# Optimization experiments

Measured on AMD Instinct MI355X. Metric: run time of the kernel, lower is better.

## Reference

```python
import jax, jax.numpy as jnp
import numpy as np

NUM_HEADS = 8
SIZE_Q = 512
SIZE_K = 512
SIZE_V = 512
B, S = 2, 2048


def setup_inputs() -> dict:
    key = jax.random.key(0)
    ks = jax.random.split(key, 16)
    Hk = SIZE_K  # num_heads * head_size_k
    Hv = SIZE_V  # num_heads * head_size_v
    inp = {
        "k": jax.random.normal(ks[0], (B, S, SIZE_K), jnp.float32),
        "v": jax.random.normal(ks[1], (B, S, SIZE_V), jnp.float32),
        "q": jax.random.normal(ks[2], (B, S, SIZE_Q), jnp.float32),
        "mask": jax.random.randint(ks[3], (S, S), 0, 2).astype(jnp.bool_),
        "spatial_bias": jax.random.normal(ks[4], (1, NUM_HEADS, S, S), jnp.float32),
        # Linear params stored as [in, out]; y = x @ W + b
        "Wq": jax.random.normal(ks[5], (SIZE_Q, Hk), jnp.float32) / np.sqrt(SIZE_Q),
        "bq": jnp.zeros((Hk,), jnp.float32),
        "Wk": jax.random.normal(ks[6], (SIZE_K, Hk), jnp.float32) / np.sqrt(SIZE_K),
        "bk": jnp.zeros((Hk,), jnp.float32),
        "Wv": jax.random.normal(ks[7], (SIZE_V, Hv), jnp.float32) / np.sqrt(SIZE_V),
        "bv": jnp.zeros((Hv,), jnp.float32),
        "Wo": jax.random.normal(ks[8], (Hv, SIZE_V), jnp.float32) / np.sqrt(Hv),
        "bo": jnp.zeros((SIZE_V,), jnp.float32),
    }
    return inp


def reference(k, v, q, mask, spatial_bias, Wq, bq, Wk, bk, Wv, bv, Wo, bo):
    batch, sk = k.shape[0], k.shape[1]
    sq = q.shape[1]
    hdk = Wk.shape[1] // NUM_HEADS
    hdv = Wv.shape[1] // NUM_HEADS
    # QKV projections -> [B, H, S, hd]
    kp = (k @ Wk + bk).reshape(batch, sk, NUM_HEADS, hdk).transpose(0, 2, 1, 3)
    vp = (v @ Wv + bv).reshape(batch, sk, NUM_HEADS, hdv).transpose(0, 2, 1, 3)
    qp = (q @ Wq + bq).reshape(batch, sq, NUM_HEADS, hdk).transpose(0, 2, 1, 3)
    qp = qp / jnp.sqrt(jnp.asarray(hdk, qp.dtype))
    # Scores with additive spatial bias and boolean mask (2D mask -> [1,1,S,S])
    scores = jnp.einsum("bhqd,bhkd->bhqk", qp, kp) + spatial_bias
    scores = jnp.where(mask[None, None, :, :], scores, -jnp.inf)
    attn = jax.nn.softmax(scores, axis=-1)  # dropout=0 (eval)
    ctx = jnp.einsum("bhqk,bhkd->bhqd", attn, vp)
    ctx = ctx.transpose(0, 2, 1, 3).reshape(batch, sq, NUM_HEADS * hdv)
    return ctx @ Wo + bo
```

## Files before the change

kernel.cpp:

```cpp
#include <hip/hip_runtime.h>
#include <hip/hip_bf16.h>

#define S_LEN 2048
#define NH 8
#define HD 64
#define CH 512
#define NEG_BIG (-3.0e38f)

typedef __bf16 bf16;
typedef bf16 bf16x8 __attribute__((ext_vector_type(8)));
typedef bf16 bf16x4 __attribute__((ext_vector_type(4)));
typedef float floatx4 __attribute__((ext_vector_type(4)));

__global__ void detect_mask_kernel(const unsigned char* __restrict__ mb,
                                   int* __restrict__ flag_out) {
    __shared__ int s1, s3;
    if (threadIdx.x == 0) { s1 = 0; s3 = 0; }
    __syncthreads();
    int any1 = 0, any3 = 0;
    int base = threadIdx.x * 16;
    for (int i = base; i < base + 16; ++i) {
        unsigned char bch = mb[i];
        int m = i & 3;
        if (bch != 0) {
            if (m == 1) any1 = 1;
            if (m == 2 || m == 3) any3 = 1;
        }
    }
    if (any1) atomicOr(&s1, 1);
    if (any3) atomicOr(&s3, 1);
    __syncthreads();
    if (threadIdx.x == 0) {
        int f = 0;
        if (s1) f = 1;
        else if (s3) f = 2;
        *flag_out = f;
    }
}

__global__ __launch_bounds__(256) void prep_weights_kernel(
    const float* __restrict__ Wq, const float* __restrict__ Wk,
    const float* __restrict__ Wv, const float* __restrict__ Wo,
    bf16* __restrict__ WThi, bf16* __restrict__ WTlo)
{
    __shared__ float tile[64][65];
    const int t = threadIdx.x;
    const int n0 = blockIdx.x * 64;
    const int k0 = blockIdx.y * 64;
    const int mat = blockIdx.z;
    const float* W = (mat == 0) ? Wq : (mat == 1) ? Wk : (mat == 2) ? Wv : Wo;
    bf16* hi = WThi + (size_t)mat * (CH * CH);
    bf16* lo = WTlo + (size_t)mat * (CH * CH);
#pragma unroll
    for (int i = 0; i < 4; ++i) {
        int row = (t >> 4) + 16 * i;
        int c4 = (t & 15) << 2;
        float4 f = *(const float4*)(W + (size_t)(k0 + row) * CH + n0 + c4);
        tile[row][c4 + 0] = f.x; tile[row][c4 + 1] = f.y;
        tile[row][c4 + 2] = f.z; tile[row][c4 + 3] = f.w;
    }
    __syncthreads();
#pragma unroll
    for (int i = 0; i < 4; ++i) {
        int nr = (t >> 4) + 16 * i;
        int k4 = (t & 15) << 2;
        bf16x4 h, l;
#pragma unroll
        for (int j = 0; j < 4; ++j) {
            float x = tile[k4 + j][nr];
            bf16 hv = (bf16)x;
            h[j] = hv;
            l[j] = (bf16)(x - (float)hv);
        }
        *(bf16x4*)(hi + (size_t)(n0 + nr) * CH + k0 + k4) = h;
        *(bf16x4*)(lo + (size_t)(n0 + nr) * CH + k0 + k4) = l;
    }
}

__device__ __forceinline__ void gemm_bf16_tile(
    bf16* __restrict__ As_hi, bf16* __restrict__ As_lo,
    bf16* __restrict__ Bs_hi, bf16* __restrict__ Bs_lo,
    const float* __restrict__ IN, const bf16* __restrict__ WThi,
    const bf16* __restrict__ WTlo, const float* __restrict__ BI,
    float* __restrict__ OUT, float scale, int mode)
{
    const int t = threadIdx.x;
    const int w = t >> 6;
    const int lane = t & 63;
    const int m16 = lane & 15;
    const int quad = lane >> 4;
    const int m0 = blockIdx.y * 128;
    const int n0 = blockIdx.x * 128;

    const int arow = t >> 1;
    const int akc  = (t & 1) << 4;

    floatx4 acc[2][8];
#pragma unroll
    for (int mi = 0; mi < 2; ++mi)
#pragma unroll
        for (int ni = 0; ni < 8; ++ni) {
            acc[mi][ni][0] = 0.f; acc[mi][ni][1] = 0.f;
            acc[mi][ni][2] = 0.f; acc[mi][ni][3] = 0.f;
        }

    float4 af[4];
    bf16x8 pbh[2], pbl[2];

    auto loadA = [&](int k0) {
        const float* p = IN + (size_t)(m0 + arow) * CH + k0 + akc;
        af[0] = ((const float4*)p)[0];
        af[1] = ((const float4*)p)[1];
        af[2] = ((const float4*)p)[2];
        af[3] = ((const float4*)p)[3];
    };
    auto loadB = [&](int k0) {
        const bf16* ph = WThi + (size_t)(n0 + arow) * CH + k0 + akc;
        const bf16* pl = WTlo + (size_t)(n0 + arow) * CH + k0 + akc;
        pbh[0] = ((const bf16x8*)ph)[0]; pbh[1] = ((const bf16x8*)ph)[1];
        pbl[0] = ((const bf16x8*)pl)[0]; pbl[1] = ((const bf16x8*)pl)[1];
    };
    auto stage = [&]() {
#pragma unroll
        for (int hh = 0; hh < 2; ++hh) {
            bf16x8 h, l;
#pragma unroll
            for (int j = 0; j < 8; ++j) {
                float x = ((const float*)&af[2 * hh])[j];
                bf16 hv = (bf16)x;
                h[j] = hv;
                l[j] = (bf16)(x - (float)hv);
            }
            *(bf16x8*)&As_hi[arow * 40 + akc + 8 * hh] = h;
            *(bf16x8*)&As_lo[arow * 40 + akc + 8 * hh] = l;
        }
        *(bf16x8*)&Bs_hi[arow * 40 + akc + 0] = pbh[0];
        *(bf16x8*)&Bs_hi[arow * 40 + akc + 8] = pbh[1];
        *(bf16x8*)&Bs_lo[arow * 40 + akc + 0] = pbl[0];
        *(bf16x8*)&Bs_lo[arow * 40 + akc + 8] = pbl[1];
    };

    loadA(0); loadB(0);
    for (int ks = 0; ks < CH / 32; ++ks) {
        __syncthreads();
        stage();
        __syncthreads();
        if (ks + 1 < CH / 32) { loadA(32 * (ks + 1)); loadB(32 * (ks + 1)); }

        bf16x8 bh[8], bl[8];
#pragma unroll
        for (int ni = 0; ni < 8; ++ni) {
            bh[ni] = *(const bf16x8*)&Bs_hi[(16 * ni + m16) * 40 + 8 * quad];
            bl[ni] = *(const bf16x8*)&Bs_lo[(16 * ni + m16) * 40 + 8 * quad];
        }
#pragma unroll
        for (int mi = 0; mi < 2; ++mi) {
            bf16x8 ah = *(const bf16x8*)&As_hi[(32 * w + 16 * mi + m16) * 40 + 8 * quad];
            bf16x8 al = *(const bf16x8*)&As_lo[(32 * w + 16 * mi + m16) * 40 + 8 * quad];
#pragma unroll
            for (int ni = 0; ni < 8; ++ni) {
                acc[mi][ni] = __builtin_amdgcn_mfma_f32_16x16x32_bf16(ah, bh[ni], acc[mi][ni], 0, 0, 0);
                acc[mi][ni] = __builtin_amdgcn_mfma_f32_16x16x32_bf16(ah, bl[ni], acc[mi][ni], 0, 0, 0);
                acc[mi][ni] = __builtin_amdgcn_mfma_f32_16x16x32_bf16(al, bh[ni], acc[mi][ni], 0, 0, 0);
            }
        }
    }

#pragma unroll
    for (int mi = 0; mi < 2; ++mi) {
#pragma unroll
        for (int r = 0; r < 4; ++r) {
            int row = m0 + 32 * w + 16 * mi + 4 * quad + r;
            int bb = row >> 11;
            int ss = row & (S_LEN - 1);
#pragma unroll
            for (int ni = 0; ni < 8; ++ni) {
                int col = n0 + 16 * ni + m16;
                float v = (acc[mi][ni][r] + BI[col]) * scale;
                if (mode == 0) {
                    int hh = col >> 6, dd = col & 63;
                    OUT[(((size_t)bb * NH + hh) * S_LEN + ss) * HD + dd] = v;
                } else if (mode == 1) {
                    int hh = col >> 6, dd = col & 63;
                    OUT[(((size_t)bb * NH + hh) * HD + dd) * S_LEN + ss] = v;
                } else {
                    OUT[(size_t)row * CH + col] = v;
                }
            }
        }
    }
}

__global__ __launch_bounds__(256, 2) void qkv_gemm_kernel(
    const float* __restrict__ q_in, const float* __restrict__ k_in,
    const float* __restrict__ v_in,
    const bf16* __restrict__ WThi, const bf16* __restrict__ WTlo,
    const float* __restrict__ bq, const float* __restrict__ bk,
    const float* __restrict__ bv,
    float* __restrict__ qp, float* __restrict__ kp, float* __restrict__ vpT)
{
    __shared__ __attribute__((aligned(16))) bf16 As_hi[128 * 40];
    __shared__ __attribute__((aligned(16))) bf16 As_lo[128 * 40];
    __shared__ __attribute__((aligned(16))) bf16 Bs_hi[128 * 40];
    __shared__ __attribute__((aligned(16))) bf16 Bs_lo[128 * 40];
    int z = blockIdx.z;
    if (z == 0)
        gemm_bf16_tile(As_hi, As_lo, Bs_hi, Bs_lo, q_in,
                       WThi, WTlo, bq, qp, 0.125f, 0);
    else if (z == 1)
        gemm_bf16_tile(As_hi, As_lo, Bs_hi, Bs_lo, k_in,
                       WThi + (size_t)CH * CH, WTlo + (size_t)CH * CH, bk, kp, 1.0f, 0);
    else
        gemm_bf16_tile(As_hi, As_lo, Bs_hi, Bs_lo, v_in,
                       WThi + (size_t)2 * CH * CH, WTlo + (size_t)2 * CH * CH, bv, vpT, 1.0f, 1);
}

__global__ __launch_bounds__(256, 2) void out_gemm_kernel(
    const float* __restrict__ ctx,
    const bf16* __restrict__ WThi, const bf16* __restrict__ WTlo,
    const float* __restrict__ bo, float* __restrict__ out)
{
    __shared__ __attribute__((aligned(16))) bf16 As_hi[128 * 40];
    __shared__ __attribute__((aligned(16))) bf16 As_lo[128 * 40];
    __shared__ __attribute__((aligned(16))) bf16 Bs_hi[128 * 40];
    __shared__ __attribute__((aligned(16))) bf16 Bs_lo[128 * 40];
    gemm_bf16_tile(As_hi, As_lo, Bs_hi, Bs_lo, ctx,
                   WThi + (size_t)3 * CH * CH, WTlo + (size_t)3 * CH * CH, bo, out, 1.0f, 2);
}

__global__ __launch_bounds__(256, 2) void attn_kernel(
    const float* __restrict__ qp, const float* __restrict__ kp,
    const float* __restrict__ vpT, const float* __restrict__ bias,
    const void* __restrict__ mask, const int* __restrict__ flagp,
    float* __restrict__ ctxb)
{
    __shared__ __attribute__((aligned(16))) bf16 Kbf[64 * 72];
    __shared__ __attribute__((aligned(16))) bf16 VsT[64 * 72];
    __shared__ __attribute__((aligned(16))) bf16 Pbf[64 * 72];
    __shared__ __attribute__((aligned(16))) float sbias[64 * 68];

    const int t    = threadIdx.x;
    const int w    = t >> 6;
    const int lane = t & 63;
    const int m    = lane & 15;
    const int quad = lane >> 4;
    const int q0   = blockIdx.x * 64;
    const int h    = blockIdx.y;
    const int b    = blockIdx.z;
    const int bh   = b * NH + h;
    const int flag = *flagp;

    bf16x8 qf[2];
    {
        const float* qrow =
            qp + ((size_t)bh * S_LEN + q0 + 16 * w + m) * HD + 8 * quad;
#pragma unroll
        for (int c = 0; c < 2; ++c) {
            float4 f0 = *(const float4*)(qrow + 32 * c);
            float4 f1 = *(const float4*)(qrow + 32 * c + 4);
            bf16x8 v;
            v[0] = (bf16)f0.x; v[1] = (bf16)f0.y; v[2] = (bf16)f0.z; v[3] = (bf16)f0.w;
            v[4] = (bf16)f1.x; v[5] = (bf16)f1.y; v[6] = (bf16)f1.z; v[7] = (bf16)f1.w;
            qf[c] = v;
        }
    }

    floatx4 ctx[4];
    float mrow[4], lrow[4];
#pragma unroll
    for (int tt = 0; tt < 4; ++tt) { ctx[tt][0]=0.f; ctx[tt][1]=0.f; ctx[tt][2]=0.f; ctx[tt][3]=0.f; }
#pragma unroll
    for (int r = 0; r < 4; ++r) { mrow[r] = NEG_BIG; lrow[r] = 0.f; }

    float4 kreg[4], vreg[4], breg[4];
    uint4  mreg[4];

    auto prefetch = [&](int k0) {
#pragma unroll
        for (int i = 0; i < 4; ++i) {
            int fl  = t + 256 * i;
            int row = fl >> 4;
            int c4  = (fl & 15) << 2;
            kreg[i] = *(const float4*)(kp  + ((size_t)bh * S_LEN + k0 + row) * HD + c4);
            vreg[i] = *(const float4*)(vpT + ((size_t)bh * HD + row) * S_LEN + k0 + c4);
            int grow = q0 + row;
            breg[i] = *(const float4*)(bias + ((size_t)h * S_LEN + grow) * S_LEN + k0 + c4);
            size_t mi0 = (size_t)grow * S_LEN + k0 + c4;
            if (flag == 1)
                mreg[i].x = *(const unsigned int*)((const unsigned char*)mask + mi0);
            else
                mreg[i] = *(const uint4*)((const unsigned int*)mask + mi0);
        }
    };
    auto stage = [&]() {
#pragma unroll
        for (int i = 0; i < 4; ++i) {
            int fl  = t + 256 * i;
            int row = fl >> 4;
            int c4  = (fl & 15) << 2;
            float4 kf = kreg[i], vf = vreg[i], bf = breg[i];
            bf16x4 kv, vv;
            kv[0] = (bf16)kf.x; kv[1] = (bf16)kf.y; kv[2] = (bf16)kf.z; kv[3] = (bf16)kf.w;
            vv[0] = (bf16)vf.x; vv[1] = (bf16)vf.y; vv[2] = (bf16)vf.z; vv[3] = (bf16)vf.w;
            *(bf16x4*)&Kbf[row * 72 + c4] = kv;
            *(bf16x4*)&VsT[row * 72 + c4] = vv;
            unsigned mj0, mj1, mj2, mj3;
            if (flag == 1) {
                unsigned mx = mreg[i].x;
                mj0 = mx & 255u; mj1 = (mx >> 8) & 255u;
                mj2 = (mx >> 16) & 255u; mj3 = mx >> 24;
            } else {
                mj0 = mreg[i].x; mj1 = mreg[i].y; mj2 = mreg[i].z; mj3 = mreg[i].w;
            }
            float4 sb;
            sb.x = mj0 ? bf.x : NEG_BIG;
            sb.y = mj1 ? bf.y : NEG_BIG;
            sb.z = mj2 ? bf.z : NEG_BIG;
            sb.w = mj3 ? bf.w : NEG_BIG;
            *(float4*)&sbias[row * 68 + c4] = sb;
        }
    };

    prefetch(0);
    for (int k0 = 0; k0 < S_LEN; k0 += 64) {
        __syncthreads();
        stage();
        __syncthreads();
        if (k0 + 64 < S_LEN) prefetch(k0 + 64);

        floatx4 sc[4];
#pragma unroll
        for (int tt = 0; tt < 4; ++tt) { sc[tt][0]=0.f; sc[tt][1]=0.f; sc[tt][2]=0.f; sc[tt][3]=0.f; }
#pragma unroll
        for (int st = 0; st < 2; ++st)
#pragma unroll
            for (int tt = 0; tt < 4; ++tt) {
                bf16x8 kf = *(const bf16x8*)&Kbf[(16 * tt + m) * 72 + 8 * quad + 32 * st];
                sc[tt] = __builtin_amdgcn_mfma_f32_16x16x32_bf16(qf[st], kf, sc[tt], 0, 0, 0);
            }

        float alpha[4];
#pragma unroll
        for (int r = 0; r < 4; ++r) {
            int lrowq = 16 * w + 4 * quad + r;
            float s[4];
#pragma unroll
            for (int tt = 0; tt < 4; ++tt)
                s[tt] = sc[tt][r] + sbias[lrowq * 68 + 16 * tt + m];
            float mx = fmaxf(fmaxf(s[0], s[1]), fmaxf(s[2], s[3]));
            mx = fmaxf(mx, __shfl_xor(mx, 1));
            mx = fmaxf(mx, __shfl_xor(mx, 2));
            mx = fmaxf(mx, __shfl_xor(mx, 4));
            mx = fmaxf(mx, __shfl_xor(mx, 8));
            float mnew = fmaxf(mrow[r], mx);
            float al = __expf(mrow[r] - mnew);
            float ls = 0.f;
#pragma unroll
            for (int tt = 0; tt < 4; ++tt) {
                float p = (s[tt] <= -1e37f) ? 0.f : __expf(s[tt] - mnew);
                ls += p;
                Pbf[lrowq * 72 + 16 * tt + m] = (bf16)p;
            }
            ls += __shfl_xor(ls, 1);
            ls += __shfl_xor(ls, 2);
            ls += __shfl_xor(ls, 4);
            ls += __shfl_xor(ls, 8);
            lrow[r] = lrow[r] * al + ls;
            mrow[r] = mnew;
            alpha[r] = al;
        }
#pragma unroll
        for (int tt = 0; tt < 4; ++tt)
#pragma unroll
            for (int r = 0; r < 4; ++r) ctx[tt][r] *= alpha[r];

#pragma unroll
        for (int st = 0; st < 2; ++st) {
            bf16x8 pf = *(const bf16x8*)&Pbf[(16 * w + m) * 72 + 8 * quad + 32 * st];
#pragma unroll
            for (int tt = 0; tt < 4; ++tt) {
                bf16x8 vf = *(const bf16x8*)&VsT[(16 * tt + m) * 72 + 8 * quad + 32 * st];
                ctx[tt] = __builtin_amdgcn_mfma_f32_16x16x32_bf16(pf, vf, ctx[tt], 0, 0, 0);
            }
        }
    }

#pragma unroll
    for (int r = 0; r < 4; ++r) {
        float inv = lrow[r] > 0.f ? 1.f / lrow[r] : 0.f;
        int grow = q0 + 16 * w + 4 * quad + r;
#pragma unroll
        for (int tt = 0; tt < 4; ++tt) {
            ctxb[((size_t)b * S_LEN + grow) * CH + h * HD + 16 * tt + m] =
                ctx[tt][r] * inv;
        }
    }
}

extern "C" void kernel_launch(void* const* d_in, const int* in_sizes, int n_in,
                              void* d_out, int out_size, void* d_ws, size_t ws_size,
                              hipStream_t stream) {
    const float* k_in = (const float*)d_in[0];
    const float* v_in = (const float*)d_in[1];
    const float* q_in = (const float*)d_in[2];
    const void*  mask = d_in[3];
    const float* bias = (const float*)d_in[4];
    const float* Wq = (const float*)d_in[5];
    const float* bq = (const float*)d_in[6];
    const float* Wk = (const float*)d_in[7];
    const float* bk = (const float*)d_in[8];
    const float* Wv = (const float*)d_in[9];
    const float* bv = (const float*)d_in[10];
    const float* Wo = (const float*)d_in[11];
    const float* bo = (const float*)d_in[12];
    float* out = (float*)d_out;

    float* wsf = (float*)d_ws;
    float* qp  = wsf;
    float* kp  = wsf + 2097152;
    float* vpT = wsf + 4194304;
    float* ctx = wsf + 6291456;
    bf16* WThi = (bf16*)(wsf + 8388608);
    bf16* WTlo = WThi + (size_t)4 * CH * CH;
    int*  flag = (int*)(WTlo + (size_t)4 * CH * CH);

    detect_mask_kernel<<<1, 256, 0, stream>>>((const unsigned char*)mask, flag);
    prep_weights_kernel<<<dim3(8, 8, 4), 256, 0, stream>>>(
        Wq, Wk, Wv, Wo, WThi, WTlo);
    qkv_gemm_kernel<<<dim3(4, 32, 3), 256, 0, stream>>>(
        q_in, k_in, v_in, WThi, WTlo, bq, bk, bv, qp, kp, vpT);
    attn_kernel<<<dim3(32, 8, 2), 256, 0, stream>>>(
        qp, kp, vpT, bias, mask, flag, ctx);
    out_gemm_kernel<<<dim3(4, 32, 1), 256, 0, stream>>>(
        ctx, WThi, WTlo, bo, out);
}
```

Before: 385.7 us.

## Store projections in bf16, premask bias to fp16, split ctx in attention

QKV projections now write bf16 outputs, with the V transpose staged through LDS for coalesced stores. A new prep kernel folds the boolean mask into the spatial bias and stores it as fp16 with a finite sentinel. The attention kernel loads compact bf16/f16 tiles, runs at higher occupancy, and emits the hi/lo bf16 split of ctx consumed directly by the output GEMM. This cuts fp32 traffic and in-loop conversion work, at the cost of an extra full pass over the bias tensor and reduced bias precision.

```diff
diff --git a/kernel.cpp b/kernel.cpp
--- a/kernel.cpp
+++ b/kernel.cpp
@@ -5,11 +5,15 @@
 #define NH 8
 #define HD 64
 #define CH 512
-#define NEG_BIG (-3.0e38f)
+#define NEG_INIT (-1.0e30f)
+#define MASK_SENT (-30000.0f)
 
 typedef __bf16 bf16;
 typedef bf16 bf16x8 __attribute__((ext_vector_type(8)));
 typedef bf16 bf16x4 __attribute__((ext_vector_type(4)));
+typedef _Float16 f16;
+typedef f16 f16x4 __attribute__((ext_vector_type(4)));
+typedef f16 f16x8 __attribute__((ext_vector_type(8)));
 typedef float floatx4 __attribute__((ext_vector_type(4)));
 
 __global__ void detect_mask_kernel(const unsigned char* __restrict__ mb,
@@ -77,18 +81,53 @@
     }
 }
 
-__device__ __forceinline__ void gemm_bf16_tile(
-    bf16* __restrict__ As_hi, bf16* __restrict__ As_lo,
-    bf16* __restrict__ Bs_hi, bf16* __restrict__ Bs_lo,
-    const float* __restrict__ IN, const bf16* __restrict__ WThi,
-    const bf16* __restrict__ WTlo, const float* __restrict__ BI,
-    float* __restrict__ OUT, float scale, int mode)
-{
+__global__ __launch_bounds__(256) void prep_sbias_kernel(
+    const float* __restrict__ bias, const void* __restrict__ mask,
+    const int* __restrict__ flagp, f16* __restrict__ sbias)
+{
+    int idx = blockIdx.x * 256 + threadIdx.x;
+    int i4 = idx << 2;
+    int q = i4 >> 11;
+    int k = i4 & (S_LEN - 1);
+    int flag = *flagp;
+    unsigned mj[4];
+    if (flag == 1) {
+        unsigned mx = *(const unsigned*)((const unsigned char*)mask + (size_t)q * S_LEN + k);
+        mj[0] = mx & 255u; mj[1] = (mx >> 8) & 255u;
+        mj[2] = (mx >> 16) & 255u; mj[3] = mx >> 24;
+    } else {
+        uint4 mx = *(const uint4*)((const unsigned*)mask + (size_t)q * S_LEN + k);
+        mj[0] = mx.x; mj[1] = mx.y; mj[2] = mx.z; mj[3] = mx.w;
+    }
+#pragma unroll
+    for (int h = 0; h < NH; ++h) {
+        float4 bv = *(const float4*)(bias + ((size_t)h * S_LEN + q) * S_LEN + k);
+        f16x4 sb;
+        sb[0] = (f16)(mj[0] ? bv.x : MASK_SENT);
+        sb[1] = (f16)(mj[1] ? bv.y : MASK_SENT);
+        sb[2] = (f16)(mj[2] ? bv.z : MASK_SENT);
+        sb[3] = (f16)(mj[3] ? bv.w : MASK_SENT);
+        *(f16x4*)(sbias + ((size_t)h * S_LEN + q) * S_LEN + k) = sb;
+    }
+}
+
+template <int MODE, bool ASPLIT>
+__device__ __forceinline__ void gemm_core(
+    bf16* __restrict__ SMEM,
+    const float* __restrict__ INF,
+    const bf16* __restrict__ INH, const bf16* __restrict__ INL,
+    const bf16* __restrict__ WThi, const bf16* __restrict__ WTlo,
+    const float* __restrict__ BI, void* __restrict__ OUT, float scale)
+{
+    bf16* As_hi = SMEM;
+    bf16* As_lo = SMEM + 128 * 40;
+    bf16* Bs_hi = SMEM + 2 * 128 * 40;
+    bf16* Bs_lo = SMEM + 3 * 128 * 40;
+
     const int t = threadIdx.x;
     const int w = t >> 6;
-    const int lane = t & 63;
-    const int m16 = lane & 15;
-    const int quad = lane >> 4;
+    const int m16 = (t & 63) & 15;
+    const int quad = (t & 63) >> 4;
     const int m0 = blockIdx.y * 128;
     const int n0 = blockIdx.x * 128;
 
@@ -105,34 +144,46 @@
         }
 
     float4 af[4];
-    bf16x8 pbh[2], pbl[2];
-
-    auto loadA = [&](int k0) {
-        const float* p = IN + (size_t)(m0 + arow) * CH + k0 + akc;
-        af[0] = ((const float4*)p)[0];
-        af[1] = ((const float4*)p)[1];
-        af[2] = ((const float4*)p)[2];
-        af[3] = ((const float4*)p)[3];
+    bf16x8 pah[2], pal[2], pbh[2], pbl[2];
+
+    auto loadA = [&](int k0c) {
+        if (ASPLIT) {
+            const bf16* ph = INH + (size_t)(m0 + arow) * CH + k0c + akc;
+            const bf16* pl = INL + (size_t)(m0 + arow) * CH + k0c + akc;
+            pah[0] = ((const bf16x8*)ph)[0]; pah[1] = ((const bf16x8*)ph)[1];
+            pal[0] = ((const bf16x8*)pl)[0]; pal[1] = ((const bf16x8*)pl)[1];
+        } else {
+            const float* p = INF + (size_t)(m0 + arow) * CH + k0c + akc;
+#pragma unroll
+            for (int i = 0; i < 4; ++i) af[i] = ((const float4*)p)[i];
+        }
     };
-    auto loadB = [&](int k0) {
-        const bf16* ph = WThi + (size_t)(n0 + arow) * CH + k0 + akc;
-        const bf16* pl = WTlo + (size_t)(n0 + arow) * CH + k0 + akc;
+    auto loadB = [&](int k0c) {
+        const bf16* ph = WThi + (size_t)(n0 + arow) * CH + k0c + akc;
+        const bf16* pl = WTlo + (size_t)(n0 + arow) * CH + k0c + akc;
         pbh[0] = ((const bf16x8*)ph)[0]; pbh[1] = ((const bf16x8*)ph)[1];
         pbl[0] = ((const bf16x8*)pl)[0]; pbl[1] = ((const bf16x8*)pl)[1];
     };
     auto stage = [&]() {
-#pragma unroll
-        for (int hh = 0; hh < 2; ++hh) {
-            bf16x8 h, l;
-#pragma unroll
-            for (int j = 0; j < 8; ++j) {
-                float x = ((const float*)&af[2 * hh])[j];
-                bf16 hv = (bf16)x;
-                h[j] = hv;
-                l[j] = (bf16)(x - (float)hv);
-            }
-            *(bf16x8*)&As_hi[arow * 40 + akc + 8 * hh] = h;
-            *(bf16x8*)&As_lo[arow * 40 + akc + 8 * hh] = l;
+        if (ASPLIT) {
+            *(bf16x8*)&As_hi[arow * 40 + akc + 0] = pah[0];
+            *(bf16x8*)&As_hi[arow * 40 + akc + 8] = pah[1];
+            *(bf16x8*)&As_lo[arow * 40 + akc + 0] = pal[0];
+            *(bf16x8*)&As_lo[arow * 40 + akc + 8] = pal[1];
+        } else {
+#pragma unroll
+            for (int hh = 0; hh < 2; ++hh) {
+                bf16x8 h, l;
+#pragma unroll
+                for (int j = 0; j < 8; ++j) {
+                    float x = ((const float*)&af[2 * hh])[j];
+                    bf16 hv = (bf16)x;
+                    h[j] = hv;
+                    l[j] = (bf16)(x - (float)hv);
+                }
+                *(bf16x8*)&As_hi[arow * 40 + akc + 8 * hh] = h;
+                *(bf16x8*)&As_lo[arow * 40 + akc + 8 * hh] = l;
+            }
         }
         *(bf16x8*)&Bs_hi[arow * 40 + akc + 0] = pbh[0];
         *(bf16x8*)&Bs_hi[arow * 40 + akc + 8] = pbh[1];
@@ -147,47 +198,71 @@
         __syncthreads();
         if (ks + 1 < CH / 32) { loadA(32 * (ks + 1)); loadB(32 * (ks + 1)); }
 
-        bf16x8 bh[8], bl[8];
+        bf16x8 ah[2], al[2];
+#pragma unroll
+        for (int mi = 0; mi < 2; ++mi) {
+            ah[mi] = *(const bf16x8*)&As_hi[(32 * w + 16 * mi + m16) * 40 + 8 * quad];
+            al[mi] = *(const bf16x8*)&As_lo[(32 * w + 16 * mi + m16) * 40 + 8 * quad];
+        }
 #pragma unroll
         for (int ni = 0; ni < 8; ++ni) {
-            bh[ni] = *(const bf16x8*)&Bs_hi[(16 * ni + m16) * 40 + 8 * quad];
-            bl[ni] = *(const bf16x8*)&Bs_lo[(16 * ni + m16) * 40 + 8 * quad];
-        }
-#pragma unroll
-        for (int mi = 0; mi < 2; ++mi) {
-            bf16x8 ah = *(const bf16x8*)&As_hi[(32 * w + 16 * mi + m16) * 40 + 8 * quad];
-            bf16x8 al = *(const bf16x8*)&As_lo[(32 * w + 16 * mi + m16) * 40 + 8 * quad];
-#pragma unroll
-            for (int ni = 0; ni < 8; ++ni) {
-                acc[mi][ni] = __builtin_amdgcn_mfma_f32_16x16x32_bf16(ah, bh[ni], acc[mi][ni], 0, 0, 0);
-                acc[mi][ni] = __builtin_amdgcn_mfma_f32_16x16x32_bf16(ah, bl[ni], acc[mi][ni], 0, 0, 0);
-                acc[mi][ni] = __builtin_amdgcn_mfma_f32_16x16x32_bf16(al, bh[ni], acc[mi][ni], 0, 0, 0);
-            }
-        }
-    }
-
-#pragma unroll
-    for (int mi = 0; mi < 2; ++mi) {
-#pragma unroll
-        for (int r = 0; r < 4; ++r) {
-            int row = m0 + 32 * w + 16 * mi + 4 * quad + r;
-            int bb = row >> 11;
-            int ss = row & (S_LEN - 1);
-#pragma unroll
-            for (int ni = 0; ni < 8; ++ni) {
-                int col = n0 + 16 * ni + m16;
-                float v = (acc[mi][ni][r] + BI[col]) * scale;
-                if (mode == 0) {
-                    int hh = col >> 6, dd = col & 63;
-                    OUT[(((size_t)bb * NH + hh) * S_LEN + ss) * HD + dd] = v;
-                } else if (mode == 1) {
-                    int hh = col >> 6, dd = col & 63;
-                    OUT[(((size_t)bb * NH + hh) * HD + dd) * S_LEN + ss] = v;
-                } else {
-                    OUT[(size_t)row * CH + col] = v;
+            bf16x8 bh = *(const bf16x8*)&Bs_hi[(16 * ni + m16) * 40 + 8 * quad];
+            bf16x8 bl = *(const bf16x8*)&Bs_lo[(16 * ni + m16) * 40 + 8 * quad];
+#pragma unroll
+            for (int mi = 0; mi < 2; ++mi) {
+                acc[mi][ni] = __builtin_amdgcn_mfma_f32_16x16x32_bf16(ah[mi], bh, acc[mi][ni], 0, 0, 0);
+                acc[mi][ni] = __builtin_amdgcn_mfma_f32_16x16x32_bf16(ah[mi], bl, acc[mi][ni], 0, 0, 0);
+                acc[mi][ni] = __builtin_amdgcn_mfma_f32_16x16x32_bf16(al[mi], bh, acc[mi][ni], 0, 0, 0);
+            }
+        }
+    }
+
+    if (MODE == 1) {
+        __syncthreads();
+        bf16* T = SMEM;
+#pragma unroll
+        for (int mi = 0; mi < 2; ++mi)
+#pragma unroll
+            for (int r = 0; r < 4; ++r) {
+                int rl = 32 * w + 16 * mi + 4 * quad + r;
+#pragma unroll
+                for (int ni = 0; ni < 8; ++ni) {
+                    int cl = 16 * ni + m16;
+                    T[cl * 136 + rl] = (bf16)(acc[mi][ni][r] + BI[n0 + cl]);
                 }
             }
-        }
+        __syncthreads();
+        int bb = m0 >> 11;
+        int s_base = m0 & (S_LEN - 1);
+        int cl = t >> 1;
+        int s_off = (t & 1) * 64;
+        int gc = n0 + cl;
+        int hh = gc >> 6, dd = gc & 63;
+        bf16* po = (bf16*)OUT +
+            (((size_t)bb * NH + hh) * HD + dd) * S_LEN + s_base + s_off;
+#pragma unroll
+        for (int j = 0; j < 8; ++j)
+            *(bf16x8*)(po + 8 * j) = *(const bf16x8*)&T[cl * 136 + s_off + 8 * j];
+    } else {
+#pragma unroll
+        for (int mi = 0; mi < 2; ++mi)
+#pragma unroll
+            for (int r = 0; r < 4; ++r) {
+                int row = m0 + 32 * w + 16 * mi + 4 * quad + r;
+                int bb = row >> 11;
+                int ss = row & (S_LEN - 1);
+#pragma unroll
+                for (int ni = 0; ni < 8; ++ni) {
+                    int col = n0 + 16 * ni + m16;
+                    float v = (acc[mi][ni][r] + BI[col]) * scale;
+                    if (MODE == 0) {
+                        int hh = col >> 6, dd = col & 63;
+                        ((bf16*)OUT)[(((size_t)bb * NH + hh) * S_LEN + ss) * HD + dd] = (bf16)v;
+                    } else {
+                        ((float*)OUT)[(size_t)row * CH + col] = v;
+                    }
+                }
+            }
     }
 }
 
@@ -197,47 +272,39 @@
     const bf16* __restrict__ WThi, const bf16* __restrict__ WTlo,
     const float* __restrict__ bq, const float* __restrict__ bk,
     const float* __restrict__ bv,
-    float* __restrict__ qp, float* __restrict__ kp, float* __restrict__ vpT)
-{
-    __shared__ __attribute__((aligned(16))) bf16 As_hi[128 * 40];
-    __shared__ __attribute__((aligned(16))) bf16 As_lo[128 * 40];
-    __shared__ __attribute__((aligned(16))) bf16 Bs_hi[128 * 40];
-    __shared__ __attribute__((aligned(16))) bf16 Bs_lo[128 * 40];
+    bf16* __restrict__ qp, bf16* __restrict__ kp, bf16* __restrict__ vpT)
+{
+    __shared__ __attribute__((aligned(16))) bf16 SMEM[4 * 128 * 40];
     int z = blockIdx.z;
     if (z == 0)
-        gemm_bf16_tile(As_hi, As_lo, Bs_hi, Bs_lo, q_in,
-                       WThi, WTlo, bq, qp, 0.125f, 0);
+        gemm_core<0, false>(SMEM, q_in, nullptr, nullptr, WThi, WTlo, bq, qp, 0.125f);
     else if (z == 1)
-        gemm_bf16_tile(As_hi, As_lo, Bs_hi, Bs_lo, k_in,
-                       WThi + (size_t)CH * CH, WTlo + (size_t)CH * CH, bk, kp, 1.0f, 0);
+        gemm_core<0, false>(SMEM, k_in, nullptr, nullptr,
+                            WThi + (size_t)CH * CH, WTlo + (size_t)CH * CH, bk, kp, 1.0f);
     else
-        gemm_bf16_tile(As_hi, As_lo, Bs_hi, Bs_lo, v_in,
-                       WThi + (size_t)2 * CH * CH, WTlo + (size_t)2 * CH * CH, bv, vpT, 1.0f, 1);
+        gemm_core<1, false>(SMEM, v_in, nullptr, nullptr,
+                            WThi + (size_t)2 * CH * CH, WTlo + (size_t)2 * CH * CH, bv, vpT, 1.0f);
 }
 
 __global__ __launch_bounds__(256, 2) void out_gemm_kernel(
-    const float* __restrict__ ctx,
+    const bf16* __restrict__ ctxhi, const bf16* __restrict__ ctxlo,
     const bf16* __restrict__ WThi, const bf16* __restrict__ WTlo,
     const float* __restrict__ bo, float* __restrict__ out)
 {
-    __shared__ __attribute__((aligned(16))) bf16 As_hi[128 * 40];
-    __shared__ __attribute__((aligned(16))) bf16 As_lo[128 * 40];
-    __shared__ __attribute__((aligned(16))) bf16 Bs_hi[128 * 40];
-    __shared__ __attribute__((aligned(16))) bf16 Bs_lo[128 * 40];
-    gemm_bf16_tile(As_hi, As_lo, Bs_hi, Bs_lo, ctx,
-                   WThi + (size_t)3 * CH * CH, WTlo + (size_t)3 * CH * CH, bo, out, 1.0f, 2);
-}
-
-__global__ __launch_bounds__(256, 2) void attn_kernel(
-    const float* __restrict__ qp, const float* __restrict__ kp,
-    const float* __restrict__ vpT, const float* __restrict__ bias,
-    const void* __restrict__ mask, const int* __restrict__ flagp,
-    float* __restrict__ ctxb)
+    __shared__ __attribute__((aligned(16))) bf16 SMEM[4 * 128 * 40];
+    gemm_core<2, true>(SMEM, nullptr, ctxhi, ctxlo,
+                       WThi + (size_t)3 * CH * CH, WTlo + (size_t)3 * CH * CH, bo, out, 1.0f);
+}
+
+__global__ __launch_bounds__(256, 4) void attn_kernel(
+    const bf16* __restrict__ qp, const bf16* __restrict__ kp,
+    const bf16* __restrict__ vpT, const f16* __restrict__ sbias,
+    bf16* __restrict__ ctxhi, bf16* __restrict__ ctxlo)
 {
     __shared__ __attribute__((aligned(16))) bf16 Kbf[64 * 72];
     __shared__ __attribute__((aligned(16))) bf16 VsT[64 * 72];
     __shared__ __attribute__((aligned(16))) bf16 Pbf[64 * 72];
-    __shared__ __attribute__((aligned(16))) float sbias[64 * 68];
+    __shared__ __attribute__((aligned(16))) f16  sb16[64 * 72];
 
     const int t    = threadIdx.x;
     const int w    = t >> 6;
@@ -248,21 +315,12 @@
     const int h    = blockIdx.y;
     const int b    = blockIdx.z;
     const int bh   = b * NH + h;
-    const int flag = *flagp;
 
     bf16x8 qf[2];
     {
-        const float* qrow =
-            qp + ((size_t)bh * S_LEN + q0 + 16 * w + m) * HD + 8 * quad;
-#pragma unroll
-        for (int c = 0; c < 2; ++c) {
-            float4 f0 = *(const float4*)(qrow + 32 * c);
-            float4 f1 = *(const float4*)(qrow + 32 * c + 4);
-            bf16x8 v;
-            v[0] = (bf16)f0.x; v[1] = (bf16)f0.y; v[2] = (bf16)f0.z; v[3] = (bf16)f0.w;
-            v[4] = (bf16)f1.x; v[5] = (bf16)f1.y; v[6] = (bf16)f1.z; v[7] = (bf16)f1.w;
-            qf[c] = v;
-        }
+        const bf16* qrow = qp + ((size_t)bh * S_LEN + q0 + 16 * w + m) * HD + 8 * quad;
+        qf[0] = *(const bf16x8*)(qrow);
+        qf[1] = *(const bf16x8*)(qrow + 32);
     }
 
     floatx4 ctx[4];
@@ -270,54 +328,31 @@
 #pragma unroll
     for (int tt = 0; tt < 4; ++tt) { ctx[tt][0]=0.f; ctx[tt][1]=0.f; ctx[tt][2]=0.f; ctx[tt][3]=0.f; }
 #pragma unroll
-    for (int r = 0; r < 4; ++r) { mrow[r] = NEG_BIG; lrow[r] = 0.f; }
-
-    float4 kreg[4], vreg[4], breg[4];
-    uint4  mreg[4];
+    for (int r = 0; r < 4; ++r) { mrow[r] = NEG_INIT; lrow[r] = 0.f; }
+
+    bf16x8 kreg[2], vreg[2];
+    f16x8  sreg[2];
 
     auto prefetch = [&](int k0) {
 #pragma unroll
-        for (int i = 0; i < 4; ++i) {
-            int fl  = t + 256 * i;
-            int row = fl >> 4;
-            int c4  = (fl & 15) << 2;
-            kreg[i] = *(const float4*)(kp  + ((size_t)bh * S_LEN + k0 + row) * HD + c4);
-            vreg[i] = *(const float4*)(vpT + ((size_t)bh * HD + row) * S_LEN + k0 + c4);
-            int grow = q0 + row;
-            breg[i] = *(const float4*)(bias + ((size_t)h * S_LEN + grow) * S_LEN + k0 + c4);
-            size_t mi0 = (size_t)grow * S_LEN + k0 + c4;
-            if (flag == 1)
-                mreg[i].x = *(const unsigned int*)((const unsigned char*)mask + mi0);
-            else
-                mreg[i] = *(const uint4*)((const unsigned int*)mask + mi0);
+        for (int i = 0; i < 2; ++i) {
+            int fl = t + 256 * i;
+            int row = fl >> 3;
+            int c8 = (fl & 7) << 3;
+            kreg[i] = *(const bf16x8*)(kp  + ((size_t)bh * S_LEN + k0 + row) * HD + c8);
+            vreg[i] = *(const bf16x8*)(vpT + ((size_t)bh * HD + row) * S_LEN + k0 + c8);
+            sreg[i] = *(const f16x8*)(sbias + ((size_t)h * S_LEN + q0 + row) * S_LEN + k0 + c8);
         }
     };
     auto stage = [&]() {
 #pragma unroll
-        for (int i = 0; i < 4; ++i) {
-            int fl  = t + 256 * i;
-            int row = fl >> 4;
-            int c4  = (fl & 15) << 2;
-            float4 kf = kreg[i], vf = vreg[i], bf = breg[i];
-            bf16x4 kv, vv;
-            kv[0] = (bf16)kf.x; kv[1] = (bf16)kf.y; kv[2] = (bf16)kf.z; kv[3] = (bf16)kf.w;
-            vv[0] = (bf16)vf.x; vv[1] = (bf16)vf.y; vv[2] = (bf16)vf.z; vv[3] = (bf16)vf.w;
-            *(bf16x4*)&Kbf[row * 72 + c4] = kv;
-            *(bf16x4*)&VsT[row * 72 + c4] = vv;
-            unsigned mj0, mj1, mj2, mj3;
-            if (flag == 1) {
-                unsigned mx = mreg[i].x;
-                mj0 = mx & 255u; mj1 = (mx >> 8) & 255u;
-                mj2 = (mx >> 16) & 255u; mj3 = mx >> 24;
-            } else {
-                mj0 = mreg[i].x; mj1 = mreg[i].y; mj2 = mreg[i].z; mj3 = mreg[i].w;
-            }
-            float4 sb;
-            sb.x = mj0 ? bf.x : NEG_BIG;
-            sb.y = mj1 ? bf.y : NEG_BIG;
-            sb.z = mj2 ? bf.z : NEG_BIG;
-            sb.w = mj3 ? bf.w : NEG_BIG;
-            *(float4*)&sbias[row * 68 + c4] = sb;
+        for (int i = 0; i < 2; ++i) {
+            int fl = t + 256 * i;
+            int row = fl >> 3;
+            int c8 = (fl & 7) << 3;
+            *(bf16x8*)&Kbf[row * 72 + c8] = kreg[i];
+            *(bf16x8*)&VsT[row * 72 + c8] = vreg[i];
+            *(f16x8*)&sb16[row * 72 + c8] = sreg[i];
         }
     };
 
@@ -346,7 +381,7 @@
             float s[4];
 #pragma unroll
             for (int tt = 0; tt < 4; ++tt)
-                s[tt] = sc[tt][r] + sbias[lrowq * 68 + 16 * tt + m];
+                s[tt] = sc[tt][r] + (float)sb16[lrowq * 72 + 16 * tt + m];
             float mx = fmaxf(fmaxf(s[0], s[1]), fmaxf(s[2], s[3]));
             mx = fmaxf(mx, __shfl_xor(mx, 1));
             mx = fmaxf(mx, __shfl_xor(mx, 2));
@@ -357,7 +392,7 @@
             float ls = 0.f;
 #pragma unroll
             for (int tt = 0; tt < 4; ++tt) {
-                float p = (s[tt] <= -1e37f) ? 0.f : __expf(s[tt] - mnew);
+                float p = (s[tt] <= -20000.f) ? 0.f : __expf(s[tt] - mnew);
                 ls += p;
                 Pbf[lrowq * 72 + 16 * tt + m] = (bf16)p;
             }
@@ -391,8 +426,11 @@
         int grow = q0 + 16 * w + 4 * quad + r;
 #pragma unroll
         for (int tt = 0; tt < 4; ++tt) {
-            ctxb[((size_t)b * S_LEN + grow) * CH + h * HD + 16 * tt + m] =
-                ctx[tt][r] * inv;
+            float v = ctx[tt][r] * inv;
+            bf16 hv = (bf16)v;
+            size_t o = ((size_t)b * S_LEN + grow) * CH + h * HD + 16 * tt + m;
+            ctxhi[o] = hv;
+            ctxlo[o] = (bf16)(v - (float)hv);
         }
     }
 }
@@ -416,21 +454,24 @@
     float* out = (float*)d_out;
 
     float* wsf = (float*)d_ws;
-    float* qp  = wsf;
-    float* kp  = wsf + 2097152;
-    float* vpT = wsf + 4194304;
-    float* ctx = wsf + 6291456;
-    bf16* WThi = (bf16*)(wsf + 8388608);
-    bf16* WTlo = WThi + (size_t)4 * CH * CH;
-    int*  flag = (int*)(WTlo + (size_t)4 * CH * CH);
+    bf16*  qp    = (bf16*)wsf;
+    bf16*  kp    = (bf16*)(wsf + 1048576);
+    bf16*  vpT   = (bf16*)(wsf + 2097152);
+    bf16*  ctxhi = (bf16*)(wsf + 3145728);
+    bf16*  ctxlo = (bf16*)(wsf + 4194304);
+    bf16*  WThi  = (bf16*)(wsf + 5242880);
+    bf16*  WTlo  = (bf16*)(wsf + 5767168);
+    int*   flag  = (int*)(wsf + 6291456);
+    f16*   sbias = (f16*)(wsf + 8388608);
 
     detect_mask_kernel<<<1, 256, 0, stream>>>((const unsigned char*)mask, flag);
     prep_weights_kernel<<<dim3(8, 8, 4), 256, 0, stream>>>(
         Wq, Wk, Wv, Wo, WThi, WTlo);
+    prep_sbias_kernel<<<4096, 256, 0, stream>>>(bias, mask, flag, sbias);
     qkv_gemm_kernel<<<dim3(4, 32, 3), 256, 0, stream>>>(
         q_in, k_in, v_in, WThi, WTlo, bq, bk, bv, qp, kp, vpT);
     attn_kernel<<<dim3(32, 8, 2), 256, 0, stream>>>(
-        qp, kp, vpT, bias, mask, flag, ctx);
-    out_gemm_kernel<<<dim3(4, 32, 1), 256, 0, stream>>>(
-        ctx, WThi, WTlo, bo, out);
-}
+        qp, kp, vpT, sbias, ctxhi, ctxlo);
+    out_gemm_kernel<<<dim3(4, 32), 256, 0, stream>>>(
+        ctxhi, ctxlo, WThi, WTlo, bo, out);
+}
```

Measured after the change: 393.3 us. Within noise of the previous version (+2.0%).
